# Kernel optimization log

Hardware: AMD Instinct MI355X
Metric: run time of the kernel (lower is better)

Reference implementation:

```python
import jax, jax.numpy as jnp
import numpy as np

B, S, D, H = 4, 8192, 1024, 16
HD = D // H  # head_dim = 64

def elu_feature_map(x):
    return jax.nn.elu(x) + 1.0

def setup_inputs() -> dict:
    key = jax.random.key(0)
    k1, k2, k3 = jax.random.split(key, 3)
    x = jax.random.normal(k1, (B, S, D), dtype=jnp.float32)
    w_qkv = jax.random.normal(k2, (3 * D, D), dtype=jnp.float32) * (D ** -0.5)
    w_out = jax.random.normal(k3, (D, D), dtype=jnp.float32) * (D ** -0.5)
    return {"x": x, "w_qkv": w_qkv, "w_out": w_out}

def reference(x, w_qkv, w_out):
    Bv, Sv, Dv = x.shape
    # qkv projection (torch Linear: x @ W.T), reshape to [3,B,H,S,hd]
    qkv = (x @ w_qkv.T).reshape(Bv, Sv, 3, H, HD)
    qkv = jnp.transpose(qkv, (2, 0, 3, 1, 4))
    q, k, v = qkv[0], qkv[1], qkv[2]
    q = elu_feature_map(q)
    k = elu_feature_map(k)
    # kv state: [B,H,hd,hd]
    kv = jnp.einsum('bhsd,bhse->bhde', k, v)
    out = jnp.einsum('bhsd,bhde->bhse', q, kv)
    k_sum = k.sum(axis=2)  # [B,H,hd]
    normalizer = jnp.einsum('bhsd,bhd->bhs', q, k_sum)[..., None]
    normalizer = jnp.maximum(normalizer, 1e-6)
    out = (out / normalizer).transpose(0, 2, 1, 3).reshape(Bv, Sv, Dv)
    return out @ w_out.T
```

## Files before the change

kernel.cpp:

```cpp
#include <hip/hip_runtime.h>
#include <cstdint>
#include <cstddef>


typedef __bf16 bf16;
typedef __bf16 bf16x8 __attribute__((ext_vector_type(8)));
typedef __bf16 bf16x4 __attribute__((ext_vector_type(4)));
typedef float  f32x4  __attribute__((ext_vector_type(4)));

#define MFMA(a, b, c) __builtin_amdgcn_mfma_f32_16x16x32_bf16((a), (b), (c), 0, 0, 0)

__device__ __forceinline__ void gld_lds16(const bf16* g, bf16* l) {
  __builtin_amdgcn_global_load_lds(
      (const __attribute__((address_space(1))) void*)g,
      (__attribute__((address_space(3))) void*)l, 16, 0, 0);
}

__global__ __launch_bounds__(256) void cvt_bf16(const float* __restrict__ src,
                                                bf16* __restrict__ dst, int n8) {
  const int stride = gridDim.x * 256;
  for (int i = blockIdx.x * 256 + threadIdx.x; i < n8; i += stride) {
    const float* p = src + (size_t)i * 8;
    f32x4 a = *(const f32x4*)p;
    f32x4 b = *(const f32x4*)(p + 4);
    bf16x8 r;
    r[0] = (bf16)a[0]; r[1] = (bf16)a[1]; r[2] = (bf16)a[2]; r[3] = (bf16)a[3];
    r[4] = (bf16)b[0]; r[5] = (bf16)b[1]; r[6] = (bf16)b[2]; r[7] = (bf16)b[3];
    *(bf16x8*)(dst + (size_t)i * 8) = r;
  }
}

template<int F32OUT>
__global__ __launch_bounds__(512, 2) void gemm_pipe(
    const bf16* __restrict__ A, const bf16* __restrict__ B,
    bf16* __restrict__ out0, bf16* __restrict__ out1,
    float* __restrict__ outf, int NC, int nelu) {
  __shared__ __align__(16) bf16 sA[3][256 * 32];
  __shared__ __align__(16) bf16 sB[3][256 * 32];
  constexpr int NT = 32;
  const int tid = threadIdx.x;
  const int w = tid >> 6, lane = tid & 63;
  const int grp = lane >> 4, mlane = lane & 15;
  const int wm = w >> 2, wn = w & 3;

  int bid = (int)blockIdx.x;
  const int cpx = (int)gridDim.x >> 3;
  bid = (bid & 7) * cpx + (bid >> 3);
  const int rt = bid / NC, ct = bid - rt * NC;
  const int rowA0 = rt * 256, colB0 = ct * 256;

  const int lr = w * 16 + (lane >> 2);
  const int lcs = (lane & 3) ^ ((lane >> 3) & 3);
  const bf16* pA = A + (size_t)(rowA0 + lr) * 1024 + lcs * 8;
  const bf16* pB = B + (size_t)(colB0 + lr) * 1024 + lcs * 8;
  const int dst = (w * 64 + lane) * 8;

  const int cgo = (grp ^ ((mlane >> 1) & 3)) * 8;
  const int arow = wm * 128 + mlane;
  const int brow = wn * 64 + mlane;

  f32x4 acc[8][4];
  const f32x4 zero = {0.f, 0.f, 0.f, 0.f};
#pragma unroll
  for (int i = 0; i < 8; ++i)
#pragma unroll
    for (int j = 0; j < 4; ++j) acc[i][j] = zero;

#pragma unroll
  for (int t = 0; t < 2; ++t) {
    const int kk = t * 32;
    bf16* a = &sA[t][0];
    bf16* b = &sB[t][0];
    gld_lds16(pA + kk, a + dst);
    gld_lds16(pB + kk, b + dst);
    gld_lds16(pA + kk + 131072, a + dst + 4096);
    gld_lds16(pB + kk + 131072, b + dst + 4096);
  }

  for (int t = 0; t < NT; ++t) {
    if (t < NT - 1) asm volatile("s_waitcnt vmcnt(4)" ::: "memory");
    else            asm volatile("s_waitcnt vmcnt(0)" ::: "memory");
    __builtin_amdgcn_s_barrier();
    __builtin_amdgcn_sched_barrier(0);

    const int bi = t % 3;
    const bf16* a = &sA[bi][0];
    const bf16* b = &sB[bi][0];
    const int ni = (t + 2) % 3;
    bf16* na = &sA[ni][0];
    bf16* nb = &sB[ni][0];
    const int kk = (t + 2) * 32;
    const bool st = (t + 2) < NT;

    bf16x8 bv[4], af[4];
#pragma unroll
    for (int nf = 0; nf < 4; ++nf)
      bv[nf] = *(const bf16x8*)&b[(brow + nf * 16) * 32 + cgo];
#pragma unroll
    for (int i = 0; i < 4; ++i)
      af[i] = *(const bf16x8*)&a[(arow + i * 16) * 32 + cgo];
    if (st) { gld_lds16(pA + kk, na + dst); gld_lds16(pB + kk, nb + dst); }
    __builtin_amdgcn_s_barrier();
    asm volatile("s_waitcnt lgkmcnt(0)" ::: "memory");
    __builtin_amdgcn_sched_barrier(0);
    __builtin_amdgcn_s_setprio(1);
#pragma unroll
    for (int i = 0; i < 4; ++i)
#pragma unroll
      for (int nf = 0; nf < 4; ++nf)
        acc[i][nf] = MFMA(af[i], bv[nf], acc[i][nf]);
    __builtin_amdgcn_s_setprio(0);
    __builtin_amdgcn_s_barrier();

#pragma unroll
    for (int i = 0; i < 4; ++i)
      af[i] = *(const bf16x8*)&a[(arow + 64 + i * 16) * 32 + cgo];
    if (st) { gld_lds16(pA + kk + 131072, na + dst + 4096);
              gld_lds16(pB + kk + 131072, nb + dst + 4096); }
    __builtin_amdgcn_s_barrier();
    asm volatile("s_waitcnt lgkmcnt(0)" ::: "memory");
    __builtin_amdgcn_sched_barrier(0);
    __builtin_amdgcn_s_setprio(1);
#pragma unroll
    for (int i = 0; i < 4; ++i)
#pragma unroll
      for (int nf = 0; nf < 4; ++nf)
        acc[4 + i][nf] = MFMA(af[i], bv[nf], acc[4 + i][nf]);
    __builtin_amdgcn_s_setprio(0);
    __builtin_amdgcn_s_barrier();
  }

  const int rbase = rowA0 + wm * 128 + grp * 4;
  const int cb0 = colB0 + wn * 64;
  if constexpr (F32OUT) {
#pragma unroll
    for (int mf = 0; mf < 8; ++mf)
#pragma unroll
      for (int nf = 0; nf < 4; ++nf) {
        float* cp = outf + (size_t)(rbase + mf * 16) * 1024 + cb0 + nf * 16 + mlane;
#pragma unroll
        for (int rr = 0; rr < 4; ++rr) cp[(size_t)rr * 1024] = acc[mf][nf][rr];
      }
  } else {
    const bool iselu = (ct < nelu);
    bf16* dp = iselu ? out0 : out1;
    const int cb = (iselu ? cb0 : cb0 - nelu * 256);
#pragma unroll
    for (int mf = 0; mf < 8; ++mf)
#pragma unroll
      for (int nf = 0; nf < 4; ++nf)
#pragma unroll
        for (int rr = 0; rr < 4; ++rr) {
          float v = acc[mf][nf][rr];
          if (iselu) v = (v > 0.f) ? (v + 1.f) : __expf(v);
          dp[(size_t)(rbase + mf * 16 + rr) * 1024 + cb + nf * 16 + mlane] = (bf16)v;
        }
  }
}

__global__ __launch_bounds__(256) void fold_kv(
    const bf16* __restrict__ kb, const bf16* __restrict__ vb,
    float* __restrict__ Pp, float* __restrict__ KsP) {
  __shared__ __align__(16) char smem[69632];
  bf16* Kt = (bf16*)smem;
  bf16* Vt = (bf16*)(smem + 34816);
  const int bh = blockIdx.x, sch = blockIdx.y;
  const int b = bh >> 4, h = bh & 15;
  const int tid = threadIdx.x, lane = tid & 63, wave = tid >> 6;
  const int grp = lane >> 4, mlane = lane & 15;
  const int rr = tid >> 3, cc = (tid & 7) * 8;

#pragma unroll
  for (int p = 0; p < 8; ++p) {
    const int r = p * 32 + rr;
    const size_t go = (size_t)(b * 8192 + sch * 256 + r) * 1024 + h * 64 + cc;
    bf16x8 k8 = *(const bf16x8*)(kb + go);
    bf16x8 v8 = *(const bf16x8*)(vb + go);
    bf16x4 klo = {k8[0], k8[1], k8[2], k8[3]}, khi = {k8[4], k8[5], k8[6], k8[7]};
    bf16x4 vlo = {v8[0], v8[1], v8[2], v8[3]}, vhi = {v8[4], v8[5], v8[6], v8[7]};
    *(bf16x4*)&Kt[r * 68 + cc] = klo;
    *(bf16x4*)&Kt[r * 68 + cc + 4] = khi;
    *(bf16x4*)&Vt[r * 68 + cc] = vlo;
    *(bf16x4*)&Vt[r * 68 + cc + 4] = vhi;
  }
  __syncthreads();

  const f32x4 zero = {0.f, 0.f, 0.f, 0.f};
  f32x4 akv[4][4], a5[4];
#pragma unroll
  for (int i = 0; i < 4; ++i) {
    a5[i] = zero;
#pragma unroll
    for (int j = 0; j < 4; ++j) akv[i][j] = zero;
  }
  bf16x8 ones;
#pragma unroll
  for (int jj = 0; jj < 8; ++jj) ones[jj] = (bf16)1.0f;

#pragma unroll
  for (int c = 0; c < 2; ++c) {
    const int sw = wave * 64 + c * 32;
    bf16x8 av[4], bk[4];
#pragma unroll
    for (int jj = 0; jj < 8; ++jj) {
      const bf16* vr = &Vt[(sw + grp * 8 + jj) * 68];
      const bf16* kr = &Kt[(sw + grp * 8 + jj) * 68];
#pragma unroll
      for (int i = 0; i < 4; ++i) av[i][jj] = vr[i * 16 + mlane];
#pragma unroll
      for (int j = 0; j < 4; ++j) bk[j][jj] = kr[j * 16 + mlane];
    }
#pragma unroll
    for (int i = 0; i < 4; ++i)
#pragma unroll
      for (int j = 0; j < 4; ++j) akv[i][j] = MFMA(av[i], bk[j], akv[i][j]);
#pragma unroll
    for (int j = 0; j < 4; ++j) a5[j] = MFMA(ones, bk[j], a5[j]);
  }
  __syncthreads();

  float* Pr = (float*)smem;
  float* Kr = (float*)(smem + 65536);
#pragma unroll
  for (int i = 0; i < 4; ++i)
#pragma unroll
    for (int j = 0; j < 4; ++j)
#pragma unroll
      for (int r = 0; r < 4; ++r)
        Pr[wave * 4096 + (i * 16 + grp * 4 + r) * 64 + j * 16 + mlane] =
            akv[i][j][r];
  if (grp == 0) {
#pragma unroll
    for (int j = 0; j < 4; ++j) Kr[wave * 64 + j * 16 + mlane] = a5[j][0];
  }
  __syncthreads();

  const int widx = bh * 32 + sch;
  float* pw = Pp + (size_t)widx * 4096;
  for (int o = tid; o < 4096; o += 256)
    pw[o] = Pr[o] + Pr[4096 + o] + Pr[8192 + o] + Pr[12288 + o];
  if (tid < 64)
    KsP[(size_t)widx * 64 + tid] =
        Kr[tid] + Kr[64 + tid] + Kr[128 + tid] + Kr[192 + tid];
}

__global__ __launch_bounds__(256) void reduce_kv2(
    const float* __restrict__ Pp, const float* __restrict__ KsP,
    bf16* __restrict__ kvb, bf16* __restrict__ ksb) {
  const int bh = blockIdx.x, y = blockIdx.y, tid = threadIdx.x;
  if (y < 16) {
    const int o = y * 256 + tid;
    const float* p = Pp + (size_t)bh * 32 * 4096 + o;
    float s = 0.f;
#pragma unroll
    for (int i = 0; i < 32; ++i) s += p[(size_t)i * 4096];
    kvb[(size_t)bh * 4096 + o] = (bf16)s;
  } else if (tid < 64) {
    const float* p = KsP + (size_t)bh * 32 * 64 + tid;
    float s = 0.f;
#pragma unroll
    for (int i = 0; i < 32; ++i) s += p[(size_t)i * 64];
    ksb[bh * 64 + tid] = (bf16)s;
  }
}

__global__ __launch_bounds__(256) void attn_k(
    const bf16* __restrict__ qb, const bf16* __restrict__ kvb,
    const bf16* __restrict__ ksb, bf16* __restrict__ attn) {
  const int bh = blockIdx.x, st = blockIdx.y;
  const int b = bh >> 4, h = bh & 15;
  const int tid = threadIdx.x, lane = tid & 63, wave = tid >> 6;
  const int grp = lane >> 4, mlane = lane & 15;
  const int s0 = st * 128, m0q = wave * 32;

  bf16x8 bkv[2][4], b5v[2];
#pragma unroll
  for (int kc = 0; kc < 2; ++kc) {
#pragma unroll
    for (int j = 0; j < 4; ++j)
      bkv[kc][j] = *(const bf16x8*)&kvb[(size_t)bh * 4096 +
                                        (j * 16 + mlane) * 64 + kc * 32 + grp * 8];
    b5v[kc] = *(const bf16x8*)&ksb[bh * 64 + kc * 32 + grp * 8];
  }

  bf16x8 aq[2][2];
#pragma unroll
  for (int kc = 0; kc < 2; ++kc)
#pragma unroll
    for (int i = 0; i < 2; ++i)
      aq[kc][i] = *(const bf16x8*)&qb[(size_t)(b * 8192 + s0 + m0q + i * 16 + mlane) * 1024 +
                                      h * 64 + kc * 32 + grp * 8];

  const f32x4 zero = {0.f, 0.f, 0.f, 0.f};
  f32x4 ao[2][4], a5[2];
#pragma unroll
  for (int i = 0; i < 2; ++i) {
    a5[i] = zero;
#pragma unroll
    for (int j = 0; j < 4; ++j) ao[i][j] = zero;
  }
#pragma unroll
  for (int kc = 0; kc < 2; ++kc)
#pragma unroll
    for (int i = 0; i < 2; ++i) {
#pragma unroll
      for (int j = 0; j < 4; ++j) ao[i][j] = MFMA(aq[kc][i], bkv[kc][j], ao[i][j]);
      a5[i] = MFMA(aq[kc][i], b5v[kc], a5[i]);
    }

#pragma unroll
  for (int i = 0; i < 2; ++i)
#pragma unroll
    for (int r = 0; r < 4; ++r) {
      const float inv = 1.0f / fmaxf(a5[i][r], 1e-6f);
      bf16* op = attn + (size_t)(b * 8192 + s0 + m0q + i * 16 + grp * 4 + r) * 1024 + h * 64;
#pragma unroll
      for (int j = 0; j < 4; ++j)
        op[j * 16 + mlane] = (bf16)(ao[i][j][r] * inv);
    }
}

extern "C" void kernel_launch(void* const* d_in, const int* in_sizes, int n_in,
                              void* d_out, int out_size, void* d_ws, size_t ws_size,
                              hipStream_t stream) {
  const float* x     = (const float*)d_in[0];
  const float* w_qkv = (const float*)d_in[1];
  const float* w_out = (const float*)d_in[2];
  char* O  = (char*)d_out;
  char* A  = (char*)d_in[0];
  char* W1 = (char*)d_in[1];

  bf16*  xb   = (bf16*)O;
  bf16*  wbq  = (bf16*)(O + 67108864);
  float* Pp   = (float*)(O + 75497472);
  float* KsP  = (float*)(O + 109051904);
  bf16*  kb   = (bf16*)A;
  bf16*  vb   = (bf16*)(A + 67108864);
  bf16*  qb   = (bf16*)A;
  bf16*  attn = (bf16*)(A + 67108864);
  bf16*  wbo  = (bf16*)W1;
  bf16*  kvb  = (bf16*)(W1 + 2097152);
  bf16*  ksb  = (bf16*)(W1 + 2621440);

  cvt_bf16<<<2048, 256, 0, stream>>>(x, xb, 4194304);
  cvt_bf16<<<1536, 256, 0, stream>>>(w_qkv, wbq, 393216);
  cvt_bf16<<<512, 256, 0, stream>>>(w_out, wbo, 131072);
  gemm_pipe<0><<<1024, 512, 0, stream>>>(xb, wbq + (size_t)1024 * 1024,
                                         kb, vb, nullptr, 8, 4);
  fold_kv<<<dim3(64, 32), 256, 0, stream>>>(kb, vb, Pp, KsP);
  reduce_kv2<<<dim3(64, 17), 256, 0, stream>>>(Pp, KsP, kvb, ksb);
  gemm_pipe<0><<<512, 512, 0, stream>>>(xb, wbq, qb, qb, nullptr, 4, 4);
  attn_k<<<dim3(64, 64), 256, 0, stream>>>(qb, kvb, ksb, attn);
  gemm_pipe<1><<<512, 512, 0, stream>>>(attn, wbo, nullptr, nullptr,
                                        (float*)O, 4, 0);
}
```

Measured before the change: 574.8 us.

## Fuse K/V projection with kv-fold and Q projection with attention apply

Replaces the separate K/V GEMM plus fold_kv with one kernel that computes a 256-row by 64-column K and V tile per head, applies ELU, stages it in LDS and folds it into the kv state without writing K/V to global memory. The Q GEMM is likewise fused with the attention-apply step, so Q stays on chip. The GEMM core moves to 256-thread blocks with 256x128 tiles, and the partial-sum reduction layout changes to match. This removes the global round-trips of K, V and Q, at the cost of smaller tiles with less reuse per block and a serialized in-block reduction.

```diff
diff --git a/kernel.cpp b/kernel.cpp
--- a/kernel.cpp
+++ b/kernel.cpp
@@ -5,7 +5,6 @@
 
 typedef __bf16 bf16;
 typedef __bf16 bf16x8 __attribute__((ext_vector_type(8)));
-typedef __bf16 bf16x4 __attribute__((ext_vector_type(4)));
 typedef float  f32x4  __attribute__((ext_vector_type(4)));
 
 #define MFMA(a, b, c) __builtin_amdgcn_mfma_f32_16x16x32_bf16((a), (b), (c), 0, 0, 0)
@@ -30,76 +29,45 @@
   }
 }
 
-template<int F32OUT>
-__global__ __launch_bounds__(512, 2) void gemm_pipe(
-    const bf16* __restrict__ A, const bf16* __restrict__ B,
-    bf16* __restrict__ out0, bf16* __restrict__ out1,
-    float* __restrict__ outf, int NC, int nelu) {
-  __shared__ __align__(16) bf16 sA[3][256 * 32];
-  __shared__ __align__(16) bf16 sB[3][256 * 32];
+__device__ __forceinline__ void kloop(
+    bf16* smem, const bf16* pA, const bf16* pB0, const bf16* pB1,
+    int tid, int arow, int brow, int cgo, f32x4 (&acc)[8][4]) {
   constexpr int NT = 32;
-  const int tid = threadIdx.x;
-  const int w = tid >> 6, lane = tid & 63;
-  const int grp = lane >> 4, mlane = lane & 15;
-  const int wm = w >> 2, wn = w & 3;
-
-  int bid = (int)blockIdx.x;
-  const int cpx = (int)gridDim.x >> 3;
-  bid = (bid & 7) * cpx + (bid >> 3);
-  const int rt = bid / NC, ct = bid - rt * NC;
-  const int rowA0 = rt * 256, colB0 = ct * 256;
-
-  const int lr = w * 16 + (lane >> 2);
-  const int lcs = (lane & 3) ^ ((lane >> 3) & 3);
-  const bf16* pA = A + (size_t)(rowA0 + lr) * 1024 + lcs * 8;
-  const bf16* pB = B + (size_t)(colB0 + lr) * 1024 + lcs * 8;
-  const int dst = (w * 64 + lane) * 8;
-
-  const int cgo = (grp ^ ((mlane >> 1) & 3)) * 8;
-  const int arow = wm * 128 + mlane;
-  const int brow = wn * 64 + mlane;
-
-  f32x4 acc[8][4];
-  const f32x4 zero = {0.f, 0.f, 0.f, 0.f};
-#pragma unroll
-  for (int i = 0; i < 8; ++i)
-#pragma unroll
-    for (int j = 0; j < 4; ++j) acc[i][j] = zero;
-
+  const int dstA = tid * 8, dstB = 8192 + tid * 8;
 #pragma unroll
   for (int t = 0; t < 2; ++t) {
+    bf16* s = smem + t * 12288;
     const int kk = t * 32;
-    bf16* a = &sA[t][0];
-    bf16* b = &sB[t][0];
-    gld_lds16(pA + kk, a + dst);
-    gld_lds16(pB + kk, b + dst);
-    gld_lds16(pA + kk + 131072, a + dst + 4096);
-    gld_lds16(pB + kk + 131072, b + dst + 4096);
-  }
-
+    gld_lds16(pA + kk,          s + dstA);
+    gld_lds16(pA + kk + 65536,  s + dstA + 2048);
+    gld_lds16(pA + kk + 131072, s + dstA + 4096);
+    gld_lds16(pA + kk + 196608, s + dstA + 6144);
+    gld_lds16(pB0 + kk,         s + dstB);
+    gld_lds16(pB1 + kk,         s + dstB + 2048);
+  }
   for (int t = 0; t < NT; ++t) {
-    if (t < NT - 1) asm volatile("s_waitcnt vmcnt(4)" ::: "memory");
+    if (t < NT - 1) asm volatile("s_waitcnt vmcnt(6)" ::: "memory");
     else            asm volatile("s_waitcnt vmcnt(0)" ::: "memory");
     __builtin_amdgcn_s_barrier();
     __builtin_amdgcn_sched_barrier(0);
 
-    const int bi = t % 3;
-    const bf16* a = &sA[bi][0];
-    const bf16* b = &sB[bi][0];
-    const int ni = (t + 2) % 3;
-    bf16* na = &sA[ni][0];
-    bf16* nb = &sB[ni][0];
+    bf16* s  = smem + (t % 3) * 12288;
+    bf16* ns = smem + ((t + 2) % 3) * 12288;
     const int kk = (t + 2) * 32;
     const bool st = (t + 2) < NT;
 
     bf16x8 bv[4], af[4];
 #pragma unroll
     for (int nf = 0; nf < 4; ++nf)
-      bv[nf] = *(const bf16x8*)&b[(brow + nf * 16) * 32 + cgo];
-#pragma unroll
-    for (int i = 0; i < 4; ++i)
-      af[i] = *(const bf16x8*)&a[(arow + i * 16) * 32 + cgo];
-    if (st) { gld_lds16(pA + kk, na + dst); gld_lds16(pB + kk, nb + dst); }
+      bv[nf] = *(const bf16x8*)&s[8192 + (brow + nf * 16) * 32 + cgo];
+#pragma unroll
+    for (int i = 0; i < 4; ++i)
+      af[i] = *(const bf16x8*)&s[(arow + i * 16) * 32 + cgo];
+    if (st) {
+      gld_lds16(pA + kk,         ns + dstA);
+      gld_lds16(pA + kk + 65536, ns + dstA + 2048);
+      gld_lds16(pB0 + kk,        ns + dstB);
+    }
     __builtin_amdgcn_s_barrier();
     asm volatile("s_waitcnt lgkmcnt(0)" ::: "memory");
     __builtin_amdgcn_sched_barrier(0);
@@ -114,9 +82,12 @@
 
 #pragma unroll
     for (int i = 0; i < 4; ++i)
-      af[i] = *(const bf16x8*)&a[(arow + 64 + i * 16) * 32 + cgo];
-    if (st) { gld_lds16(pA + kk + 131072, na + dst + 4096);
-              gld_lds16(pB + kk + 131072, nb + dst + 4096); }
+      af[i] = *(const bf16x8*)&s[(arow + 64 + i * 16) * 32 + cgo];
+    if (st) {
+      gld_lds16(pA + kk + 131072, ns + dstA + 4096);
+      gld_lds16(pA + kk + 196608, ns + dstA + 6144);
+      gld_lds16(pB1 + kk,         ns + dstB + 2048);
+    }
     __builtin_amdgcn_s_barrier();
     asm volatile("s_waitcnt lgkmcnt(0)" ::: "memory");
     __builtin_amdgcn_sched_barrier(0);
@@ -129,63 +100,58 @@
     __builtin_amdgcn_s_setprio(0);
     __builtin_amdgcn_s_barrier();
   }
-
-  const int rbase = rowA0 + wm * 128 + grp * 4;
-  const int cb0 = colB0 + wn * 64;
-  if constexpr (F32OUT) {
+}
+
+__global__ __launch_bounds__(256, 2) void gemm_kvfold(
+    const bf16* __restrict__ xb, const bf16* __restrict__ wbq,
+    float* __restrict__ Pp, float* __restrict__ KsP) {
+  __shared__ __align__(16) bf16 smem[36864];
+  const int tid = threadIdx.x;
+  const int w = tid >> 6, lane = tid & 63;
+  const int grp = lane >> 4, mlane = lane & 15;
+  const int wm = w >> 1, wn = w & 1;
+
+  int bid = (int)blockIdx.x;
+  const int cpx = (int)gridDim.x >> 3;
+  bid = (bid & 7) * cpx + (bid >> 3);
+  const int h = bid & 15, rt = bid >> 4;
+  const int rowA0 = rt * 256;
+
+  const int lrr = tid >> 2;
+  const int lcs = (tid & 3) ^ ((tid >> 3) & 3);
+  const bf16* pA  = xb + (size_t)(rowA0 + lrr) * 1024 + lcs * 8;
+  const bf16* pB0 = wbq + (size_t)(1024 + h * 64 + lrr) * 1024 + lcs * 8;
+  const bf16* pB1 = wbq + (size_t)(2048 + h * 64 + lrr) * 1024 + lcs * 8;
+  const int cgo = (grp ^ ((mlane >> 1) & 3)) * 8;
+  const int arow = wm * 128 + mlane;
+  const int brow = wn * 64 + mlane;
+
+  const f32x4 zero = {0.f, 0.f, 0.f, 0.f};
+  f32x4 acc[8][4];
+#pragma unroll
+  for (int i = 0; i < 8; ++i)
+#pragma unroll
+    for (int j = 0; j < 4; ++j) acc[i][j] = zero;
+
+  kloop(smem, pA, pB0, pB1, tid, arow, brow, cgo, acc);
+
+  bf16* Kt = smem;
+  bf16* Vt = smem + 17408;
+  {
+    bf16* T = wn ? Vt : Kt;
 #pragma unroll
     for (int mf = 0; mf < 8; ++mf)
 #pragma unroll
-      for (int nf = 0; nf < 4; ++nf) {
-        float* cp = outf + (size_t)(rbase + mf * 16) * 1024 + cb0 + nf * 16 + mlane;
-#pragma unroll
-        for (int rr = 0; rr < 4; ++rr) cp[(size_t)rr * 1024] = acc[mf][nf][rr];
-      }
-  } else {
-    const bool iselu = (ct < nelu);
-    bf16* dp = iselu ? out0 : out1;
-    const int cb = (iselu ? cb0 : cb0 - nelu * 256);
-#pragma unroll
-    for (int mf = 0; mf < 8; ++mf)
-#pragma unroll
       for (int nf = 0; nf < 4; ++nf)
 #pragma unroll
-        for (int rr = 0; rr < 4; ++rr) {
-          float v = acc[mf][nf][rr];
-          if (iselu) v = (v > 0.f) ? (v + 1.f) : __expf(v);
-          dp[(size_t)(rbase + mf * 16 + rr) * 1024 + cb + nf * 16 + mlane] = (bf16)v;
+        for (int r = 0; r < 4; ++r) {
+          float v = acc[mf][nf][r];
+          if (wn == 0) v = (v > 0.f) ? (v + 1.f) : __expf(v);
+          T[(wm * 128 + mf * 16 + grp * 4 + r) * 68 + nf * 16 + mlane] = (bf16)v;
         }
   }
-}
-
-__global__ __launch_bounds__(256) void fold_kv(
-    const bf16* __restrict__ kb, const bf16* __restrict__ vb,
-    float* __restrict__ Pp, float* __restrict__ KsP) {
-  __shared__ __align__(16) char smem[69632];
-  bf16* Kt = (bf16*)smem;
-  bf16* Vt = (bf16*)(smem + 34816);
-  const int bh = blockIdx.x, sch = blockIdx.y;
-  const int b = bh >> 4, h = bh & 15;
-  const int tid = threadIdx.x, lane = tid & 63, wave = tid >> 6;
-  const int grp = lane >> 4, mlane = lane & 15;
-  const int rr = tid >> 3, cc = (tid & 7) * 8;
-
-#pragma unroll
-  for (int p = 0; p < 8; ++p) {
-    const int r = p * 32 + rr;
-    const size_t go = (size_t)(b * 8192 + sch * 256 + r) * 1024 + h * 64 + cc;
-    bf16x8 k8 = *(const bf16x8*)(kb + go);
-    bf16x8 v8 = *(const bf16x8*)(vb + go);
-    bf16x4 klo = {k8[0], k8[1], k8[2], k8[3]}, khi = {k8[4], k8[5], k8[6], k8[7]};
-    bf16x4 vlo = {v8[0], v8[1], v8[2], v8[3]}, vhi = {v8[4], v8[5], v8[6], v8[7]};
-    *(bf16x4*)&Kt[r * 68 + cc] = klo;
-    *(bf16x4*)&Kt[r * 68 + cc + 4] = khi;
-    *(bf16x4*)&Vt[r * 68 + cc] = vlo;
-    *(bf16x4*)&Vt[r * 68 + cc + 4] = vhi;
-  }
   __syncthreads();
 
-  const f32x4 zero = {0.f, 0.f, 0.f, 0.f};
   f32x4 akv[4][4], a5[4];
 #pragma unroll
   for (int i = 0; i < 4; ++i) {
@@ -199,7 +165,7 @@
 
 #pragma unroll
   for (int c = 0; c < 2; ++c) {
-    const int sw = wave * 64 + c * 32;
+    const int sw = w * 64 + c * 32;
     bf16x8 av[4], bk[4];
 #pragma unroll
     for (int jj = 0; jj < 8; ++jj) {
@@ -220,103 +186,231 @@
   __syncthreads();
 
   float* Pr = (float*)smem;
-  float* Kr = (float*)(smem + 65536);
-#pragma unroll
-  for (int i = 0; i < 4; ++i)
-#pragma unroll
-    for (int j = 0; j < 4; ++j)
-#pragma unroll
-      for (int r = 0; r < 4; ++r)
-        Pr[wave * 4096 + (i * 16 + grp * 4 + r) * 64 + j * 16 + mlane] =
-            akv[i][j][r];
-  if (grp == 0) {
-#pragma unroll
-    for (int j = 0; j < 4; ++j) Kr[wave * 64 + j * 16 + mlane] = a5[j][0];
+  float* Kr = Pr + 8192;
+  if (w >= 2) {
+#pragma unroll
+    for (int i = 0; i < 4; ++i)
+#pragma unroll
+      for (int j = 0; j < 4; ++j)
+#pragma unroll
+        for (int r = 0; r < 4; ++r)
+          Pr[(w - 2) * 4096 + (i * 16 + grp * 4 + r) * 64 + j * 16 + mlane] =
+              akv[i][j][r];
+    if (grp == 0) {
+#pragma unroll
+      for (int j = 0; j < 4; ++j) Kr[(w - 2) * 64 + j * 16 + mlane] = a5[j][0];
+    }
   }
   __syncthreads();
-
-  const int widx = bh * 32 + sch;
-  float* pw = Pp + (size_t)widx * 4096;
-  for (int o = tid; o < 4096; o += 256)
-    pw[o] = Pr[o] + Pr[4096 + o] + Pr[8192 + o] + Pr[12288 + o];
-  if (tid < 64)
-    KsP[(size_t)widx * 64 + tid] =
-        Kr[tid] + Kr[64 + tid] + Kr[128 + tid] + Kr[192 + tid];
+  if (w < 2) {
+#pragma unroll
+    for (int i = 0; i < 4; ++i)
+#pragma unroll
+      for (int j = 0; j < 4; ++j)
+#pragma unroll
+        for (int r = 0; r < 4; ++r)
+          akv[i][j][r] += Pr[w * 4096 + (i * 16 + grp * 4 + r) * 64 + j * 16 + mlane];
+    if (grp == 0) {
+#pragma unroll
+      for (int j = 0; j < 4; ++j) a5[j][0] += Kr[w * 64 + j * 16 + mlane];
+    }
+  }
+  __syncthreads();
+  if (w == 1) {
+#pragma unroll
+    for (int i = 0; i < 4; ++i)
+#pragma unroll
+      for (int j = 0; j < 4; ++j)
+#pragma unroll
+        for (int r = 0; r < 4; ++r)
+          Pr[(i * 16 + grp * 4 + r) * 64 + j * 16 + mlane] = akv[i][j][r];
+    if (grp == 0) {
+#pragma unroll
+      for (int j = 0; j < 4; ++j) Kr[j * 16 + mlane] = a5[j][0];
+    }
+  }
+  __syncthreads();
+  if (w == 0) {
+    const int widx = rt * 16 + h;
+    float* pw = Pp + (size_t)widx * 4096;
+#pragma unroll
+    for (int i = 0; i < 4; ++i)
+#pragma unroll
+      for (int j = 0; j < 4; ++j)
+#pragma unroll
+        for (int r = 0; r < 4; ++r)
+          pw[(i * 16 + grp * 4 + r) * 64 + j * 16 + mlane] =
+              akv[i][j][r] + Pr[(i * 16 + grp * 4 + r) * 64 + j * 16 + mlane];
+    if (grp == 0) {
+#pragma unroll
+      for (int j = 0; j < 4; ++j)
+        KsP[(size_t)widx * 64 + j * 16 + mlane] =
+            a5[j][0] + Kr[j * 16 + mlane];
+    }
+  }
 }
 
 __global__ __launch_bounds__(256) void reduce_kv2(
     const float* __restrict__ Pp, const float* __restrict__ KsP,
     bf16* __restrict__ kvb, bf16* __restrict__ ksb) {
   const int bh = blockIdx.x, y = blockIdx.y, tid = threadIdx.x;
+  const int b = bh >> 4, h = bh & 15;
   if (y < 16) {
     const int o = y * 256 + tid;
-    const float* p = Pp + (size_t)bh * 32 * 4096 + o;
     float s = 0.f;
 #pragma unroll
-    for (int i = 0; i < 32; ++i) s += p[(size_t)i * 4096];
+    for (int i = 0; i < 32; ++i)
+      s += Pp[(size_t)((b * 32 + i) * 16 + h) * 4096 + o];
     kvb[(size_t)bh * 4096 + o] = (bf16)s;
   } else if (tid < 64) {
-    const float* p = KsP + (size_t)bh * 32 * 64 + tid;
     float s = 0.f;
 #pragma unroll
-    for (int i = 0; i < 32; ++i) s += p[(size_t)i * 64];
+    for (int i = 0; i < 32; ++i)
+      s += KsP[(size_t)((b * 32 + i) * 16 + h) * 64 + tid];
     ksb[bh * 64 + tid] = (bf16)s;
   }
 }
 
-__global__ __launch_bounds__(256) void attn_k(
-    const bf16* __restrict__ qb, const bf16* __restrict__ kvb,
-    const bf16* __restrict__ ksb, bf16* __restrict__ attn) {
-  const int bh = blockIdx.x, st = blockIdx.y;
-  const int b = bh >> 4, h = bh & 15;
-  const int tid = threadIdx.x, lane = tid & 63, wave = tid >> 6;
+__global__ __launch_bounds__(256, 2) void gemm_qattn(
+    const bf16* __restrict__ xb, const bf16* __restrict__ wbq,
+    const bf16* __restrict__ kvb, const bf16* __restrict__ ksb,
+    bf16* __restrict__ attn) {
+  __shared__ __align__(16) bf16 smem[36864];
+  const int tid = threadIdx.x;
+  const int w = tid >> 6, lane = tid & 63;
   const int grp = lane >> 4, mlane = lane & 15;
-  const int s0 = st * 128, m0q = wave * 32;
-
+  const int wm = w >> 1, wn = w & 1;
+
+  int bid = (int)blockIdx.x;
+  const int cpx = (int)gridDim.x >> 3;
+  bid = (bid & 7) * cpx + (bid >> 3);
+  const int ct = bid & 7, rt = bid >> 3;
+  const int rowA0 = rt * 256;
+
+  const int lrr = tid >> 2;
+  const int lcs = (tid & 3) ^ ((tid >> 3) & 3);
+  const bf16* pA  = xb + (size_t)(rowA0 + lrr) * 1024 + lcs * 8;
+  const bf16* pB0 = wbq + (size_t)(ct * 128 + lrr) * 1024 + lcs * 8;
+  const bf16* pB1 = pB0 + (size_t)64 * 1024;
+  const int cgo = (grp ^ ((mlane >> 1) & 3)) * 8;
+  const int arow = wm * 128 + mlane;
+  const int brow = wn * 64 + mlane;
+
+  const f32x4 zero = {0.f, 0.f, 0.f, 0.f};
+  f32x4 acc[8][4];
+#pragma unroll
+  for (int i = 0; i < 8; ++i)
+#pragma unroll
+    for (int j = 0; j < 4; ++j) acc[i][j] = zero;
+
+  kloop(smem, pA, pB0, pB1, tid, arow, brow, cgo, acc);
+
+  const int head = ct * 2 + wn;
+  const int bh = (rt >> 5) * 16 + head;
   bf16x8 bkv[2][4], b5v[2];
 #pragma unroll
-  for (int kc = 0; kc < 2; ++kc) {
-#pragma unroll
-    for (int j = 0; j < 4; ++j)
-      bkv[kc][j] = *(const bf16x8*)&kvb[(size_t)bh * 4096 +
-                                        (j * 16 + mlane) * 64 + kc * 32 + grp * 8];
-    b5v[kc] = *(const bf16x8*)&ksb[bh * 64 + kc * 32 + grp * 8];
-  }
-
-  bf16x8 aq[2][2];
-#pragma unroll
-  for (int kc = 0; kc < 2; ++kc)
-#pragma unroll
-    for (int i = 0; i < 2; ++i)
-      aq[kc][i] = *(const bf16x8*)&qb[(size_t)(b * 8192 + s0 + m0q + i * 16 + mlane) * 1024 +
-                                      h * 64 + kc * 32 + grp * 8];
+  for (int ks = 0; ks < 2; ++ks) {
+#pragma unroll
+    for (int nf = 0; nf < 4; ++nf)
+      bkv[ks][nf] = *(const bf16x8*)&kvb[(size_t)bh * 4096 +
+                                         (nf * 16 + mlane) * 64 + ks * 32 + grp * 8];
+    b5v[ks] = *(const bf16x8*)&ksb[bh * 64 + ks * 32 + grp * 8];
+  }
+
+  bf16* Qs = smem + w * 4096;
+  const int swr = (mlane >> 1) & 7;
+#pragma unroll
+  for (int mh = 0; mh < 2; ++mh) {
+#pragma unroll
+    for (int i = 0; i < 4; ++i)
+#pragma unroll
+      for (int nf = 0; nf < 4; ++nf)
+#pragma unroll
+        for (int r = 0; r < 4; ++r) {
+          float v = acc[mh * 4 + i][nf][r];
+          v = (v > 0.f) ? (v + 1.f) : __expf(v);
+          const int rw = i * 16 + grp * 4 + r;
+          const int d = nf * 16 + mlane;
+          Qs[rw * 64 + (((d >> 3) ^ ((rw >> 1) & 7)) << 3) + (d & 7)] = (bf16)v;
+        }
+    bf16x8 aq2[4][2];
+#pragma unroll
+    for (int i = 0; i < 4; ++i)
+#pragma unroll
+      for (int ks = 0; ks < 2; ++ks)
+        aq2[i][ks] = *(const bf16x8*)&Qs[(i * 16 + mlane) * 64 +
+                                         (((ks * 4 + grp) ^ swr) << 3)];
+    f32x4 ao[4][4], a5q[4];
+#pragma unroll
+    for (int i = 0; i < 4; ++i) {
+      a5q[i] = zero;
+#pragma unroll
+      for (int nf = 0; nf < 4; ++nf) ao[i][nf] = zero;
+    }
+#pragma unroll
+    for (int ks = 0; ks < 2; ++ks)
+#pragma unroll
+      for (int i = 0; i < 4; ++i) {
+#pragma unroll
+        for (int nf = 0; nf < 4; ++nf)
+          ao[i][nf] = MFMA(aq2[i][ks], bkv[ks][nf], ao[i][nf]);
+        a5q[i] = MFMA(aq2[i][ks], b5v[ks], a5q[i]);
+      }
+#pragma unroll
+    for (int i = 0; i < 4; ++i)
+#pragma unroll
+      for (int r = 0; r < 4; ++r) {
+        const float inv = 1.0f / fmaxf(a5q[i][r], 1e-6f);
+        bf16* op = attn + (size_t)(rowA0 + wm * 128 + mh * 64 + i * 16 +
+                                   grp * 4 + r) * 1024 + head * 64;
+#pragma unroll
+        for (int nf = 0; nf < 4; ++nf)
+          op[nf * 16 + mlane] = (bf16)(ao[i][nf][r] * inv);
+      }
+  }
+}
+
+__global__ __launch_bounds__(256, 2) void gemm_out(
+    const bf16* __restrict__ attn, const bf16* __restrict__ wbo,
+    float* __restrict__ C) {
+  __shared__ __align__(16) bf16 smem[36864];
+  const int tid = threadIdx.x;
+  const int w = tid >> 6, lane = tid & 63;
+  const int grp = lane >> 4, mlane = lane & 15;
+  const int wm = w >> 1, wn = w & 1;
+
+  int bid = (int)blockIdx.x;
+  const int cpx = (int)gridDim.x >> 3;
+  bid = (bid & 7) * cpx + (bid >> 3);
+  const int ct = bid & 7, rt = bid >> 3;
+  const int rowA0 = rt * 256;
+
+  const int lrr = tid >> 2;
+  const int lcs = (tid & 3) ^ ((tid >> 3) & 3);
+  const bf16* pA  = attn + (size_t)(rowA0 + lrr) * 1024 + lcs * 8;
+  const bf16* pB0 = wbo + (size_t)(ct * 128 + lrr) * 1024 + lcs * 8;
+  const bf16* pB1 = pB0 + (size_t)64 * 1024;
+  const int cgo = (grp ^ ((mlane >> 1) & 3)) * 8;
+  const int arow = wm * 128 + mlane;
+  const int brow = wn * 64 + mlane;
 
   const f32x4 zero = {0.f, 0.f, 0.f, 0.f};
-  f32x4 ao[2][4], a5[2];
-#pragma unroll
-  for (int i = 0; i < 2; ++i) {
-    a5[i] = zero;
-#pragma unroll
-    for (int j = 0; j < 4; ++j) ao[i][j] = zero;
-  }
-#pragma unroll
-  for (int kc = 0; kc < 2; ++kc)
-#pragma unroll
-    for (int i = 0; i < 2; ++i) {
-#pragma unroll
-      for (int j = 0; j < 4; ++j) ao[i][j] = MFMA(aq[kc][i], bkv[kc][j], ao[i][j]);
-      a5[i] = MFMA(aq[kc][i], b5v[kc], a5[i]);
-    }
-
-#pragma unroll
-  for (int i = 0; i < 2; ++i)
-#pragma unroll
-    for (int r = 0; r < 4; ++r) {
-      const float inv = 1.0f / fmaxf(a5[i][r], 1e-6f);
-      bf16* op = attn + (size_t)(b * 8192 + s0 + m0q + i * 16 + grp * 4 + r) * 1024 + h * 64;
-#pragma unroll
-      for (int j = 0; j < 4; ++j)
-        op[j * 16 + mlane] = (bf16)(ao[i][j][r] * inv);
+  f32x4 acc[8][4];
+#pragma unroll
+  for (int i = 0; i < 8; ++i)
+#pragma unroll
+    for (int j = 0; j < 4; ++j) acc[i][j] = zero;
+
+  kloop(smem, pA, pB0, pB1, tid, arow, brow, cgo, acc);
+
+#pragma unroll
+  for (int mf = 0; mf < 8; ++mf)
+#pragma unroll
+    for (int nf = 0; nf < 4; ++nf) {
+      float* cp = C + (size_t)(rowA0 + wm * 128 + mf * 16 + grp * 4) * 1024 +
+                  ct * 128 + wn * 64 + nf * 16 + mlane;
+#pragma unroll
+      for (int r = 0; r < 4; ++r) cp[(size_t)r * 1024] = acc[mf][nf][r];
     }
 }
 
@@ -334,10 +428,7 @@
   bf16*  wbq  = (bf16*)(O + 67108864);
   float* Pp   = (float*)(O + 75497472);
   float* KsP  = (float*)(O + 109051904);
-  bf16*  kb   = (bf16*)A;
-  bf16*  vb   = (bf16*)(A + 67108864);
-  bf16*  qb   = (bf16*)A;
-  bf16*  attn = (bf16*)(A + 67108864);
+  bf16*  attn = (bf16*)A;
   bf16*  wbo  = (bf16*)W1;
   bf16*  kvb  = (bf16*)(W1 + 2097152);
   bf16*  ksb  = (bf16*)(W1 + 2621440);
@@ -345,12 +436,8 @@
   cvt_bf16<<<2048, 256, 0, stream>>>(x, xb, 4194304);
   cvt_bf16<<<1536, 256, 0, stream>>>(w_qkv, wbq, 393216);
   cvt_bf16<<<512, 256, 0, stream>>>(w_out, wbo, 131072);
-  gemm_pipe<0><<<1024, 512, 0, stream>>>(xb, wbq + (size_t)1024 * 1024,
-                                         kb, vb, nullptr, 8, 4);
-  fold_kv<<<dim3(64, 32), 256, 0, stream>>>(kb, vb, Pp, KsP);
+  gemm_kvfold<<<2048, 256, 0, stream>>>(xb, wbq, Pp, KsP);
   reduce_kv2<<<dim3(64, 17), 256, 0, stream>>>(Pp, KsP, kvb, ksb);
-  gemm_pipe<0><<<512, 512, 0, stream>>>(xb, wbq, qb, qb, nullptr, 4, 4);
-  attn_k<<<dim3(64, 64), 256, 0, stream>>>(qb, kvb, ksb, attn);
-  gemm_pipe<1><<<512, 512, 0, stream>>>(attn, wbo, nullptr, nullptr,
-                                        (float*)O, 4, 0);
-}
+  gemm_qattn<<<1024, 256, 0, stream>>>(xb, wbq, kvb, ksb, attn);
+  gemm_out<<<1024, 256, 0, stream>>>(attn, wbo, (float*)O);
+}
```

Result: faster. 538.0 us (-6.4%).
